# Kernel optimization log

Measured on AMD Instinct MI355X. Metric: run time of the kernel, lower is better.

Reference implementation:

```python
import jax, jax.numpy as jnp
import numpy as np

B, S, D = 4, 2048, 1024


def setup_inputs() -> dict:
    key = jax.random.key(0)
    ks = jax.random.split(key, 9)
    scale = 1.0 / np.sqrt(D)
    v = jax.random.normal(ks[0], (B, S, D), dtype=jnp.float32)
    k = jax.random.normal(ks[1], (B, S, D), dtype=jnp.float32)
    q = jax.random.normal(ks[2], (B, S, D), dtype=jnp.float32)
    # causal boolean mask broadcast over batch: [B, S, S]
    mask = jnp.broadcast_to(jnp.tril(jnp.ones((S, S), dtype=bool)), (B, S, S))
    Wq = jax.random.normal(ks[3], (D, D), dtype=jnp.float32) * scale
    bq = jnp.zeros((D,), dtype=jnp.float32)
    Wk = jax.random.normal(ks[4], (D, D), dtype=jnp.float32) * scale
    bk = jnp.zeros((D,), dtype=jnp.float32)
    Wv = jax.random.normal(ks[5], (D, D), dtype=jnp.float32) * scale
    bv = jnp.zeros((D,), dtype=jnp.float32)
    return {"v": v, "k": k, "q": q, "mask": mask,
            "Wq": Wq, "bq": bq, "Wk": Wk, "bk": bk, "Wv": Wv, "bv": bv}


def reference(v, k, q, mask, Wq, bq, Wk, bk, Wv, bv):
    # Dense projections (flax Dense: x @ W + b)
    qp = jnp.einsum('bsd,de->bse', q, Wq) + bq
    kp = jnp.einsum('bsd,de->bse', k, Wk) + bk
    vp = jnp.einsum('bsd,de->bse', v, Wv) + bv
    inv_sqrt_d = jnp.float32(1.0 / np.sqrt(D))
    scores = jnp.einsum('bqd,bkd->bqk', qp, kp) * inv_sqrt_d  # [B,S,S]
    scores = jnp.where(mask, scores, jnp.float32(-1e10))
    attn = jax.nn.softmax(scores, axis=-1)
    return qp + jnp.einsum('bqk,bkd->bqd', attn, vp)
```

## Files before the change

kernel.cpp:

```cpp
#include <hip/hip_runtime.h>
#include <hip/hip_bf16.h>
#include <stdint.h>
#include <stddef.h>


using bf16 = __hip_bfloat16;
typedef __attribute__((ext_vector_type(8))) short short8;
typedef __attribute__((ext_vector_type(4))) float f32x4;

#define B_ 4
#define S_ 2048
#define D_ 1024
#define NTOK (B_ * S_)
#define NELEM ((size_t)NTOK * D_)

__device__ __forceinline__ float bits_to_f(unsigned short h) {
  union { unsigned int u; float f; } c;
  c.u = ((unsigned int)h) << 16;
  return c.f;
}

__device__ __forceinline__ void gld_lds16(const void* g, void* l) {
  __builtin_amdgcn_global_load_lds(
      (const __attribute__((address_space(1))) unsigned int*)g,
      (__attribute__((address_space(3))) unsigned int*)l, 16, 0, 0);
}

__global__ void detect_kernel(const unsigned short* __restrict__ qraw,
                              int* __restrict__ flag) {
  const int lane = threadIdx.x;
  const float v = fabsf(bits_to_f(qraw[2 * lane]));
  const bool sane = (v < 64.0f) && (v == 0.0f || v > 1e-30f);
  const unsigned long long m = __ballot(sane);
  if (lane == 0) *flag = (__popcll(m) >= 56) ? 1 : 0;
}

__global__ __launch_bounds__(256) void prep_kernel(
    const void* __restrict__ v, const void* __restrict__ k,
    const void* __restrict__ q,
    const void* __restrict__ Wq, const void* __restrict__ Wk,
    const void* __restrict__ Wv,
    bf16* __restrict__ X, bf16* __restrict__ WT,
    float* __restrict__ rowsum, const int* __restrict__ flag)
{
  __shared__ bf16 tbuf[32][33];
  const int bid = blockIdx.x;
  const int tid = threadIdx.x;
  const int mode = *flag;

  if (bid < 12288) {
    const int z = bid >> 12;
    const void* src = (z == 0) ? v : (z == 1) ? k : q;
    bf16* d = X + (size_t)z * NELEM;
    const size_t i = (size_t)(bid & 4095) * 256 + tid;
    if (mode) {
      ((uint4*)d)[i] = ((const uint4*)src)[i];
    } else {
      const float4 a = ((const float4*)src)[2 * i];
      const float4 b = ((const float4*)src)[2 * i + 1];
      __align__(16) bf16 t[8];
      t[0] = __float2bfloat16(a.x); t[1] = __float2bfloat16(a.y);
      t[2] = __float2bfloat16(a.z); t[3] = __float2bfloat16(a.w);
      t[4] = __float2bfloat16(b.x); t[5] = __float2bfloat16(b.y);
      t[6] = __float2bfloat16(b.z); t[7] = __float2bfloat16(b.w);
      ((uint4*)d)[i] = *(const uint4*)t;
    }
  } else if (bid < 15360) {
    const int t = bid - 12288;
    const int z = t >> 10;
    const int tt = t & 1023;
    const void* W = (z == 0) ? Wq : (z == 1) ? Wk : Wv;
    bf16* O = WT + (size_t)z * D_ * D_;
    const int bx = (tt & 31) * 32, by = (tt >> 5) * 32;
    const int tx = tid & 31, ty = tid >> 5;
#pragma unroll
    for (int i = 0; i < 32; i += 8) {
      const size_t idx = (size_t)(by + ty + i) * D_ + bx + tx;
      const float val = mode ? __bfloat162float(((const bf16*)W)[idx])
                             : ((const float*)W)[idx];
      tbuf[ty + i][tx] = __float2bfloat16(val);
    }
    __syncthreads();
#pragma unroll
    for (int i = 0; i < 32; i += 8)
      O[(size_t)(bx + ty + i) * D_ + by + tx] = tbuf[tx][ty + i];
  } else {
    rowsum[(bid - 15360) * 256 + tid] = 0.f;
  }
}

__device__ __forceinline__ void gemm_core(
    const bf16* __restrict__ A, int lda, int m0,
    const bf16* __restrict__ Bt, int ldb, int n0,
    int kEnd, bf16* As, bf16* Bs, f32x4 acc[4][4])
{
  const int tid  = threadIdx.x;
  const int wave = tid >> 6;
  const int lane = tid & 63;
  const int wr = wave >> 2;
  const int wc = wave & 3;
  const int fr = lane & 15;
  const int q4 = lane >> 4;
  const int nt = kEnd >> 6;

  const int srow = tid >> 2;
  const int sxq  = ((tid & 3) ^ (srow & 3)) * 8;
  const bf16* Asrc  = A  + (size_t)(m0 + srow) * lda + sxq;
  const bf16* Bsrc0 = Bt + (size_t)(n0 + srow) * ldb + sxq;
  const bf16* Bsrc1 = Bt + (size_t)(n0 + 128 + srow) * ldb + sxq;
  const int wofs = wave * 512;

  const int fxq  = (q4 ^ (fr & 3)) * 8;
  const int aoff = (wr * 64 + fr) * 32 + fxq;
  const int boff = (wc * 64 + fr) * 32 + fxq;

#define STAGE_HALF(tt_, h_) do {                                          \
    const int t_ = (tt_);                                                 \
    const int tc = (t_ < nt) ? t_ : (nt - 1);      \
    const int kb = (tc << 6) + (h_) * 32;                                 \
    const int ab = ((t_ & 1) * 2 + (h_)) * 4096;                          \
    const int bb = ((t_ & 1) * 2 + (h_)) * 8192;                          \
    gld_lds16(Asrc  + kb, As + ab + wofs);                                \
    gld_lds16(Bsrc0 + kb, Bs + bb + wofs);                                \
    gld_lds16(Bsrc1 + kb, Bs + bb + 4096 + wofs);                         \
  } while (0)

  STAGE_HALF(0, 0); STAGE_HALF(0, 1); STAGE_HALF(1, 0);
  asm volatile("s_waitcnt vmcnt(6)" ::: "memory");
  __builtin_amdgcn_s_barrier();

  for (int t = 0; t < nt; ++t) {
    const int b = t & 1;
#pragma unroll
    for (int h = 0; h < 2; ++h) {
      const int abase = (b * 2 + h) * 4096 + aoff;
      const int bbase = (b * 2 + h) * 8192 + boff;
      short8 af[4], bg[4];
#pragma unroll
      for (int i = 0; i < 4; ++i) {
        af[i] = *(const short8*)(As + abase + i * 512);
        bg[i] = *(const short8*)(Bs + bbase + i * 512);
      }
      if (h == 0) STAGE_HALF(t + 1, 1);
      else        STAGE_HALF(t + 2, 0);
      asm volatile("s_waitcnt vmcnt(6)" ::: "memory");
      __builtin_amdgcn_s_barrier();
      asm volatile("s_waitcnt lgkmcnt(0)" ::: "memory");
      __builtin_amdgcn_sched_barrier(0);
      __builtin_amdgcn_s_setprio(1);
#pragma unroll
      for (int mi = 0; mi < 4; ++mi)
#pragma unroll
        for (int ni = 0; ni < 4; ++ni)
          acc[mi][ni] = __builtin_amdgcn_mfma_f32_16x16x32_bf16(
              af[mi], bg[ni], acc[mi][ni], 0, 0, 0);
      __builtin_amdgcn_s_setprio(0);
      __builtin_amdgcn_s_barrier();
    }
  }
  asm volatile("s_waitcnt vmcnt(0)" ::: "memory");
#undef STAGE_HALF
}

__global__ __launch_bounds__(512) void proj_kernel(
    const bf16* __restrict__ xc,
    const bf16* __restrict__ WT,
    const void* __restrict__ bq, const void* __restrict__ bk,
    const void* __restrict__ bv,
    bf16* __restrict__ qp, bf16* __restrict__ kp, bf16* __restrict__ vpt,
    const int* __restrict__ flag)
{
  __shared__ bf16 As[16384];
  __shared__ bf16 Bs[32768];

  int lin = blockIdx.x + 64 * (blockIdx.y + 4 * blockIdx.z);
  lin = (lin & 7) * 96 + (lin >> 3);
  const int bx = lin & 63;
  const int by = (lin >> 6) & 3;
  const int z  = lin >> 8;

  const bf16* Act  = xc + (size_t)(z == 0 ? 2 : (z == 1 ? 1 : 0)) * NELEM;
  const void* bias = (z == 0) ? bq : (z == 1) ? bk : bv;
  const bf16* Bmat = WT + (size_t)z * D_ * D_;
  const int m0 = bx * 128, n0 = by * 256;

  f32x4 acc[4][4] = {};
  gemm_core(Act, D_, m0, Bmat, D_, n0, D_, As, Bs, acc);

  const int mode = *flag;
  const int lane = threadIdx.x & 63, wave = threadIdx.x >> 6;
  const int wr = wave >> 2, wc = wave & 3;
  const int fr = lane & 15, q4 = lane >> 4;
#pragma unroll
  for (int ni = 0; ni < 4; ++ni) {
    const int n = n0 + wc * 64 + ni * 16 + fr;
    const float bval = mode ? __bfloat162float(((const bf16*)bias)[n])
                            : ((const float*)bias)[n];
#pragma unroll
    for (int mi = 0; mi < 4; ++mi)
#pragma unroll
      for (int i = 0; i < 4; ++i) {
        const int m = m0 + wr * 64 + mi * 16 + q4 * 4 + i;
        const float val = acc[mi][ni][i] + bval;
        if (z == 0)      qp[(size_t)m * D_ + n] = __float2bfloat16(val);
        else if (z == 1) kp[(size_t)m * D_ + n] = __float2bfloat16(val);
        else {
          const int b = m >> 11, s = m & (S_ - 1);
          vpt[((size_t)b * D_ + n) * S_ + s] = __float2bfloat16(val);
        }
      }
  }
}

__global__ __launch_bounds__(512) void scores_kernel(
    const bf16* __restrict__ qp, const bf16* __restrict__ kp,
    bf16* __restrict__ sc, float* __restrict__ rowsum)
{
  const int m0 = blockIdx.x * 128, n0 = blockIdx.y * 256, bb = blockIdx.z;
  if (n0 > m0 + 127) return;
  __shared__ bf16 As[16384];
  __shared__ bf16 Bs[32768];
  const bf16* A  = qp + (size_t)bb * S_ * D_;
  const bf16* Bt = kp + (size_t)bb * S_ * D_;

  f32x4 acc[4][4] = {};
  gemm_core(A, D_, m0, Bt, D_, n0, D_, As, Bs, acc);

  bf16* out = sc + (size_t)bb * S_ * S_;
  float* rs = rowsum + (size_t)bb * S_;
  const float scale = 0.03125f;
  const float MAXS = 8.0f;
  const int lane = threadIdx.x & 63, wave = threadIdx.x >> 6;
  const int wr = wave >> 2, wc = wave & 3;
  const int fr = lane & 15, q4 = lane >> 4;
#pragma unroll
  for (int mi = 0; mi < 4; ++mi) {
#pragma unroll
    for (int i = 0; i < 4; ++i) {
      const int m = m0 + wr * 64 + mi * 16 + q4 * 4 + i;
      float part = 0.f;
#pragma unroll
      for (int ni = 0; ni < 4; ++ni) {
        const int n = n0 + wc * 64 + ni * 16 + fr;
        float p = 0.f;
        if (n <= m) {
          const bf16 pb = __float2bfloat16(__expf(acc[mi][ni][i] * scale - MAXS));
          p = __bfloat162float(pb);
          out[(size_t)m * S_ + n] = pb;
        } else {
          out[(size_t)m * S_ + n] = __float2bfloat16(0.f);
        }
        part += p;
      }
      part += __shfl_down(part, 8, 64);
      part += __shfl_down(part, 4, 64);
      part += __shfl_down(part, 2, 64);
      part += __shfl_down(part, 1, 64);
      if (fr == 0) atomicAdd(&rs[m], part);
    }
  }
}

__global__ __launch_bounds__(512) void pv_kernel(
    const bf16* __restrict__ attn, const bf16* __restrict__ vpt,
    const bf16* __restrict__ qp, const float* __restrict__ rowsum,
    void* __restrict__ out, const int* __restrict__ flag)
{
  __shared__ bf16 As[16384];
  __shared__ bf16 Bs[32768];
  const int m0 = (15 - blockIdx.x) * 128;
  const int n0 = blockIdx.y * 256, bb = blockIdx.z;
  const bf16* A  = attn + (size_t)bb * S_ * S_;
  const bf16* Bt = vpt  + (size_t)bb * D_ * S_;

  f32x4 acc[4][4] = {};
  gemm_core(A, S_, m0, Bt, S_, n0, m0 + 128, As, Bs, acc);

  const int mode = *flag;
  const bf16* qpb = qp + (size_t)bb * S_ * D_;
  const float* rs = rowsum + (size_t)bb * S_;
  const size_t obase = (size_t)bb * S_ * D_;
  const int lane = threadIdx.x & 63, wave = threadIdx.x >> 6;
  const int wr = wave >> 2, wc = wave & 3;
  const int fr = lane & 15, q4 = lane >> 4;
#pragma unroll
  for (int mi = 0; mi < 4; ++mi)
#pragma unroll
    for (int i = 0; i < 4; ++i) {
      const int m = m0 + wr * 64 + mi * 16 + q4 * 4 + i;
      const float inv = 1.f / rs[m];
#pragma unroll
      for (int ni = 0; ni < 4; ++ni) {
        const int n = n0 + wc * 64 + ni * 16 + fr;
        const float val = acc[mi][ni][i] * inv +
                          __bfloat162float(qpb[(size_t)m * D_ + n]);
        const size_t idx = obase + (size_t)m * D_ + n;
        if (mode) ((bf16*)out)[idx] = __float2bfloat16(val);
        else      ((float*)out)[idx] = val;
      }
    }
}

extern "C" void kernel_launch(void* const* d_in, const int* in_sizes, int n_in,
                              void* d_out, int out_size, void* d_ws, size_t ws_size,
                              hipStream_t stream) {
  (void)in_sizes; (void)n_in; (void)out_size; (void)ws_size;
  const void* v  = d_in[0];
  const void* k  = d_in[1];
  const void* q  = d_in[2];
  const void* Wq = d_in[4];
  const void* bq = d_in[5];
  const void* Wk = d_in[6];
  const void* bk = d_in[7];
  const void* Wv = d_in[8];
  const void* bv = d_in[9];

  char* ws = (char*)d_ws;
  int*   flag   = (int*)ws;           ws += 256;
  float* rowsum = (float*)ws;         ws += (size_t)NTOK * 4;
  bf16* WT   = (bf16*)ws;             ws += (size_t)3 * D_ * D_ * 2;
  bf16* qp   = (bf16*)ws;             ws += NELEM * 2;
  bf16* kp   = (bf16*)ws;             ws += NELEM * 2;
  bf16* vpt  = (bf16*)ws;             ws += NELEM * 2;
  bf16* X    = (bf16*)ws;
  bf16* sc   = X;

  detect_kernel<<<dim3(1), dim3(64), 0, stream>>>((const unsigned short*)q, flag);
  prep_kernel<<<dim3(15392), dim3(256), 0, stream>>>(
      v, k, q, Wq, Wk, Wv, X, WT, rowsum, flag);
  proj_kernel<<<dim3(64, 4, 3), dim3(512), 0, stream>>>(
      X, WT, bq, bk, bv, qp, kp, vpt, flag);
  scores_kernel<<<dim3(16, 8, 4), dim3(512), 0, stream>>>(qp, kp, sc, rowsum);
  pv_kernel<<<dim3(16, 4, 4), dim3(512), 0, stream>>>(
      sc, vpt, qp, rowsum, d_out, flag);
}
```

Before: 401.4 us.

## Enlarge GEMM tiles to 256x256 with full-K64 staging and 8x4 accumulators

Rewrites the shared GEMM core to use 256x256 block tiles: each wave now computes 128x64 with 8x4 MFMA accumulators, and a full 64-wide K tile is staged per iteration with an 8-way XOR swizzle. This replaces the half-tile three-stage pipeline with simpler double buffering. The block swizzle in the projection kernel is dropped and all three GEMM kernels get half as many blocks along M. The goal is more operand reuse per LDS load and fewer global loads, but it costs more registers and LDS (128KB per block), gives coarser causal skipping and fewer blocks to fill the GPU, and the pipeline is less finely overlapped.

```diff
diff --git a/kernel.cpp b/kernel.cpp
--- a/kernel.cpp
+++ b/kernel.cpp
@@ -92,7 +92,7 @@
 __device__ __forceinline__ void gemm_core(
     const bf16* __restrict__ A, int lda, int m0,
     const bf16* __restrict__ Bt, int ldb, int n0,
-    int kEnd, bf16* As, bf16* Bs, f32x4 acc[4][4])
+    int kEnd, bf16* As, bf16* Bs, f32x4 acc[8][4])
 {
   const int tid  = threadIdx.x;
   const int wave = tid >> 6;
@@ -103,66 +103,62 @@
   const int q4 = lane >> 4;
   const int nt = kEnd >> 6;
 
-  const int srow = tid >> 2;
-  const int sxq  = ((tid & 3) ^ (srow & 3)) * 8;
-  const bf16* Asrc  = A  + (size_t)(m0 + srow) * lda + sxq;
-  const bf16* Bsrc0 = Bt + (size_t)(n0 + srow) * ldb + sxq;
-  const bf16* Bsrc1 = Bt + (size_t)(n0 + 128 + srow) * ldb + sxq;
+  const int trow = tid >> 3;
+  const int tsw  = ((tid & 7) ^ (trow & 7)) * 8;
+  const bf16* Asrc = A  + (size_t)(m0 + trow) * lda + tsw;
+  const bf16* Bsrc = Bt + (size_t)(n0 + trow) * ldb + tsw;
   const int wofs = wave * 512;
 
-  const int fxq  = (q4 ^ (fr & 3)) * 8;
-  const int aoff = (wr * 64 + fr) * 32 + fxq;
-  const int boff = (wc * 64 + fr) * 32 + fxq;
-
-#define STAGE_HALF(tt_, h_) do {                                          \
-    const int t_ = (tt_);                                                 \
-    const int tc = (t_ < nt) ? t_ : (nt - 1);      \
-    const int kb = (tc << 6) + (h_) * 32;                                 \
-    const int ab = ((t_ & 1) * 2 + (h_)) * 4096;                          \
-    const int bb = ((t_ & 1) * 2 + (h_)) * 8192;                          \
-    gld_lds16(Asrc  + kb, As + ab + wofs);                                \
-    gld_lds16(Bsrc0 + kb, Bs + bb + wofs);                                \
-    gld_lds16(Bsrc1 + kb, Bs + bb + 4096 + wofs);                         \
+  const int co0 = (q4 ^ (fr & 7)) * 8;
+  const int abase0 = (wr * 128 + fr) * 64;
+  const int bbase0 = (wc * 64 + fr) * 64;
+
+#define STAGE_TILE(tt_) do {                                              \
+    const int kb_ = (tt_) << 6;                                           \
+    const int bo_ = (((tt_) & 1) << 14) + wofs;                           \
+    _Pragma("unroll")                                                     \
+    for (int i_ = 0; i_ < 4; ++i_) {                                      \
+      gld_lds16(Asrc + (size_t)(i_ * 64) * lda + kb_, As + bo_ + i_ * 4096); \
+      gld_lds16(Bsrc + (size_t)(i_ * 64) * ldb + kb_, Bs + bo_ + i_ * 4096); \
+    }                                                                     \
   } while (0)
 
-  STAGE_HALF(0, 0); STAGE_HALF(0, 1); STAGE_HALF(1, 0);
-  asm volatile("s_waitcnt vmcnt(6)" ::: "memory");
-  __builtin_amdgcn_s_barrier();
+  STAGE_TILE(0);
+  __syncthreads();
 
   for (int t = 0; t < nt; ++t) {
-    const int b = t & 1;
+    if (t + 1 < nt) STAGE_TILE(t + 1);
+    const int ab = ((t & 1) << 14) + abase0;
+    const int bb = ((t & 1) << 14) + bbase0;
 #pragma unroll
     for (int h = 0; h < 2; ++h) {
-      const int abase = (b * 2 + h) * 4096 + aoff;
-      const int bbase = (b * 2 + h) * 8192 + boff;
-      short8 af[4], bg[4];
-#pragma unroll
-      for (int i = 0; i < 4; ++i) {
-        af[i] = *(const short8*)(As + abase + i * 512);
-        bg[i] = *(const short8*)(Bs + bbase + i * 512);
+      const int co = co0 ^ (h << 5);
+      short8 bg[4];
+#pragma unroll
+      for (int ni = 0; ni < 4; ++ni)
+        bg[ni] = *(const short8*)(Bs + bb + ni * 1024 + co);
+#pragma unroll
+      for (int mh = 0; mh < 2; ++mh) {
+        short8 af[4];
+#pragma unroll
+        for (int j = 0; j < 4; ++j)
+          af[j] = *(const short8*)(As + ab + (mh * 4 + j) * 1024 + co);
+        __builtin_amdgcn_s_setprio(1);
+#pragma unroll
+        for (int j = 0; j < 4; ++j)
+#pragma unroll
+          for (int ni = 0; ni < 4; ++ni)
+            acc[mh * 4 + j][ni] = __builtin_amdgcn_mfma_f32_16x16x32_bf16(
+                af[j], bg[ni], acc[mh * 4 + j][ni], 0, 0, 0);
+        __builtin_amdgcn_s_setprio(0);
       }
-      if (h == 0) STAGE_HALF(t + 1, 1);
-      else        STAGE_HALF(t + 2, 0);
-      asm volatile("s_waitcnt vmcnt(6)" ::: "memory");
-      __builtin_amdgcn_s_barrier();
-      asm volatile("s_waitcnt lgkmcnt(0)" ::: "memory");
-      __builtin_amdgcn_sched_barrier(0);
-      __builtin_amdgcn_s_setprio(1);
-#pragma unroll
-      for (int mi = 0; mi < 4; ++mi)
-#pragma unroll
-        for (int ni = 0; ni < 4; ++ni)
-          acc[mi][ni] = __builtin_amdgcn_mfma_f32_16x16x32_bf16(
-              af[mi], bg[ni], acc[mi][ni], 0, 0, 0);
-      __builtin_amdgcn_s_setprio(0);
-      __builtin_amdgcn_s_barrier();
-    }
+    }
+    __syncthreads();
   }
-  asm volatile("s_waitcnt vmcnt(0)" ::: "memory");
-#undef STAGE_HALF
-}
-
-__global__ __launch_bounds__(512) void proj_kernel(
+#undef STAGE_TILE
+}
+
+__global__ __launch_bounds__(512, 2) void proj_kernel(
     const bf16* __restrict__ xc,
     const bf16* __restrict__ WT,
     const void* __restrict__ bq, const void* __restrict__ bk,
@@ -170,21 +166,15 @@
     bf16* __restrict__ qp, bf16* __restrict__ kp, bf16* __restrict__ vpt,
     const int* __restrict__ flag)
 {
-  __shared__ bf16 As[16384];
+  __shared__ bf16 As[32768];
   __shared__ bf16 Bs[32768];
-
-  int lin = blockIdx.x + 64 * (blockIdx.y + 4 * blockIdx.z);
-  lin = (lin & 7) * 96 + (lin >> 3);
-  const int bx = lin & 63;
-  const int by = (lin >> 6) & 3;
-  const int z  = lin >> 8;
-
+  const int z = blockIdx.z;
   const bf16* Act  = xc + (size_t)(z == 0 ? 2 : (z == 1 ? 1 : 0)) * NELEM;
   const void* bias = (z == 0) ? bq : (z == 1) ? bk : bv;
   const bf16* Bmat = WT + (size_t)z * D_ * D_;
-  const int m0 = bx * 128, n0 = by * 256;
-
-  f32x4 acc[4][4] = {};
+  const int m0 = blockIdx.x * 256, n0 = blockIdx.y * 256;
+
+  f32x4 acc[8][4] = {};
   gemm_core(Act, D_, m0, Bmat, D_, n0, D_, As, Bs, acc);
 
   const int mode = *flag;
@@ -197,10 +187,10 @@
     const float bval = mode ? __bfloat162float(((const bf16*)bias)[n])
                             : ((const float*)bias)[n];
 #pragma unroll
-    for (int mi = 0; mi < 4; ++mi)
+    for (int mi = 0; mi < 8; ++mi)
 #pragma unroll
       for (int i = 0; i < 4; ++i) {
-        const int m = m0 + wr * 64 + mi * 16 + q4 * 4 + i;
+        const int m = m0 + wr * 128 + mi * 16 + q4 * 4 + i;
         const float val = acc[mi][ni][i] + bval;
         if (z == 0)      qp[(size_t)m * D_ + n] = __float2bfloat16(val);
         else if (z == 1) kp[(size_t)m * D_ + n] = __float2bfloat16(val);
@@ -212,18 +202,18 @@
   }
 }
 
-__global__ __launch_bounds__(512) void scores_kernel(
+__global__ __launch_bounds__(512, 2) void scores_kernel(
     const bf16* __restrict__ qp, const bf16* __restrict__ kp,
     bf16* __restrict__ sc, float* __restrict__ rowsum)
 {
-  const int m0 = blockIdx.x * 128, n0 = blockIdx.y * 256, bb = blockIdx.z;
-  if (n0 > m0 + 127) return;
-  __shared__ bf16 As[16384];
+  if (blockIdx.y > blockIdx.x) return;
+  const int m0 = blockIdx.x * 256, n0 = blockIdx.y * 256, bb = blockIdx.z;
+  __shared__ bf16 As[32768];
   __shared__ bf16 Bs[32768];
   const bf16* A  = qp + (size_t)bb * S_ * D_;
   const bf16* Bt = kp + (size_t)bb * S_ * D_;
 
-  f32x4 acc[4][4] = {};
+  f32x4 acc[8][4] = {};
   gemm_core(A, D_, m0, Bt, D_, n0, D_, As, Bs, acc);
 
   bf16* out = sc + (size_t)bb * S_ * S_;
@@ -234,10 +224,10 @@
   const int wr = wave >> 2, wc = wave & 3;
   const int fr = lane & 15, q4 = lane >> 4;
 #pragma unroll
-  for (int mi = 0; mi < 4; ++mi) {
+  for (int mi = 0; mi < 8; ++mi) {
 #pragma unroll
     for (int i = 0; i < 4; ++i) {
-      const int m = m0 + wr * 64 + mi * 16 + q4 * 4 + i;
+      const int m = m0 + wr * 128 + mi * 16 + q4 * 4 + i;
       float part = 0.f;
 #pragma unroll
       for (int ni = 0; ni < 4; ++ni) {
@@ -261,20 +251,20 @@
   }
 }
 
-__global__ __launch_bounds__(512) void pv_kernel(
+__global__ __launch_bounds__(512, 2) void pv_kernel(
     const bf16* __restrict__ attn, const bf16* __restrict__ vpt,
     const bf16* __restrict__ qp, const float* __restrict__ rowsum,
     void* __restrict__ out, const int* __restrict__ flag)
 {
-  __shared__ bf16 As[16384];
+  __shared__ bf16 As[32768];
   __shared__ bf16 Bs[32768];
-  const int m0 = (15 - blockIdx.x) * 128;
+  const int m0 = (7 - blockIdx.x) * 256;
   const int n0 = blockIdx.y * 256, bb = blockIdx.z;
   const bf16* A  = attn + (size_t)bb * S_ * S_;
   const bf16* Bt = vpt  + (size_t)bb * D_ * S_;
 
-  f32x4 acc[4][4] = {};
-  gemm_core(A, S_, m0, Bt, S_, n0, m0 + 128, As, Bs, acc);
+  f32x4 acc[8][4] = {};
+  gemm_core(A, S_, m0, Bt, S_, n0, m0 + 256, As, Bs, acc);
 
   const int mode = *flag;
   const bf16* qpb = qp + (size_t)bb * S_ * D_;
@@ -284,10 +274,10 @@
   const int wr = wave >> 2, wc = wave & 3;
   const int fr = lane & 15, q4 = lane >> 4;
 #pragma unroll
-  for (int mi = 0; mi < 4; ++mi)
+  for (int mi = 0; mi < 8; ++mi)
 #pragma unroll
     for (int i = 0; i < 4; ++i) {
-      const int m = m0 + wr * 64 + mi * 16 + q4 * 4 + i;
+      const int m = m0 + wr * 128 + mi * 16 + q4 * 4 + i;
       const float inv = 1.f / rs[m];
 #pragma unroll
       for (int ni = 0; ni < 4; ++ni) {
@@ -328,9 +318,9 @@
   detect_kernel<<<dim3(1), dim3(64), 0, stream>>>((const unsigned short*)q, flag);
   prep_kernel<<<dim3(15392), dim3(256), 0, stream>>>(
       v, k, q, Wq, Wk, Wv, X, WT, rowsum, flag);
-  proj_kernel<<<dim3(64, 4, 3), dim3(512), 0, stream>>>(
+  proj_kernel<<<dim3(32, 4, 3), dim3(512), 0, stream>>>(
       X, WT, bq, bk, bv, qp, kp, vpt, flag);
-  scores_kernel<<<dim3(16, 8, 4), dim3(512), 0, stream>>>(qp, kp, sc, rowsum);
-  pv_kernel<<<dim3(16, 4, 4), dim3(512), 0, stream>>>(
+  scores_kernel<<<dim3(8, 8, 4), dim3(512), 0, stream>>>(qp, kp, sc, rowsum);
+  pv_kernel<<<dim3(8, 4, 4), dim3(512), 0, stream>>>(
       sc, vpt, qp, rowsum, d_out, flag);
 }
```

Measured after the change: 433.2 us. 7.9% more time.
